# Performance work log

Measured on AMD Instinct MI355X. Metric: run time of the kernel, lower is better.

The kernel has to match this reference:

```python
import jax, jax.numpy as jnp
import numpy as np

WIRES = 4
LAYERS = 3
B = 1024
P = 14 * 14  # 196 patches


def setup_inputs() -> dict:
    key = jax.random.key(0)
    k1, k2, k3 = jax.random.split(key, 3)
    x = jax.random.uniform(k1, (B, 1, 28, 28), jnp.float32)
    q_params = jax.random.normal(k2, (LAYERS, WIRES), jnp.float32)
    W = jax.random.normal(k3, (10, 4 * 14 * 14), jnp.float32) * 0.02
    b = jnp.zeros((10,), jnp.float32)
    return {"x": x, "q_params": q_params, "W": W, "b": b}


def _cnot(state, ctrl, tgt):
    # state: [B,P,2,2,2,2]; wire w lives on axis 2+w
    c_ax, t_ax = 2 + ctrl, 2 + tgt
    s0, s1 = jnp.split(state, 2, axis=c_ax)
    s1 = jnp.flip(s1, axis=t_ax)  # flip target when control=1
    return jnp.concatenate([s0, s1], axis=c_ax)


def _circuit(xp, q_params):
    # xp: [B,P,4] RX angles per wire. Returns <Z_w> per wire: [B,P,4].
    Bn, Pn = xp.shape[0], xp.shape[1]
    state = jnp.zeros((Bn, Pn, 2, 2, 2, 2), jnp.complex64).at[:, :, 0, 0, 0, 0].set(1.0)
    for i in range(LAYERS):
        # RX(x[w]) on each wire (angle varies per batch/patch)
        for w in range(WIRES):
            half = xp[:, :, w] * 0.5
            c = jnp.cos(half).astype(jnp.complex64)
            s = (-1j) * jnp.sin(half).astype(jnp.complex64)
            mat = jnp.stack([jnp.stack([c, s], -1), jnp.stack([s, c], -1)], -2)  # [B,P,2,2]
            st = jnp.moveaxis(state, 2 + w, -1)
            st = jnp.einsum('BPij,BPuvwj->BPuvwi', mat, st)
            state = jnp.moveaxis(st, -1, 2 + w)
        state = _cnot(state, 0, 1)
        state = _cnot(state, 2, 3)
        # RZ(params[i,w]) on each wire (scalar phase, diagonal gate)
        for w in range(WIRES):
            phi = q_params[i, w].astype(jnp.complex64)
            ph = jnp.stack([jnp.exp(-0.5j * phi), jnp.exp(0.5j * phi)])  # [2]
            st = jnp.moveaxis(state, 2 + w, -1) * ph
            state = jnp.moveaxis(st, -1, 2 + w)
    probs = state.real ** 2 + state.imag ** 2  # [B,P,2,2,2,2]
    zs = []
    for w in range(WIRES):
        axes = tuple(a for a in range(2, 6) if a != 2 + w)
        m = probs.sum(axes)  # [B,P,2]
        zs.append(m[..., 0] - m[..., 1])
    return jnp.stack(zs, -1)  # [B,P,4]


def reference(x, q_params, W, b):
    Bn = x.shape[0]
    # 2x2 patches in row-major (r,c) order; per-patch flatten order matches
    # view of x[:,0,r:r+2,c:c+2]: [tl, tr, bl, br]
    xp = x[:, 0].reshape(Bn, 14, 2, 14, 2).transpose(0, 1, 3, 2, 4).reshape(Bn, P, 4)
    z = _circuit(xp, q_params)            # [B,196,4]
    feats = z.reshape(Bn, P * 4).astype(jnp.float32)  # cat order: patch-major, wire-minor
    logits = feats @ W.T + b
    return jax.nn.log_softmax(logits, axis=-1)
```

## Files before the change

kernel.cpp:

```cpp
#include <hip/hip_runtime.h>
#include <math.h>

#define WIRES   4
#define LAYERS  3
#define PATCHES 196

__global__ __launch_bounds__(256) void quanv_fused(
    const float* __restrict__ x,
    const float* __restrict__ qp,
    const float* __restrict__ Wt,
    const float* __restrict__ bias,
    float* __restrict__ out)
{
    __shared__ float phr[LAYERS][16];
    __shared__ float phim[LAYERS][16];
    __shared__ float wsum[4][10];
    __shared__ float lg[10];

    const int b = blockIdx.x;
    const int t = threadIdx.x;

    float cw[4], sw[4];
    if (t < PATCHES) {
        const int r = t / 14, cc = t % 14;
        const float* xb = x + (size_t)b * 784;
        const float2 top = *reinterpret_cast<const float2*>(xb + (2 * r) * 28 + 2 * cc);
        const float2 bot = *reinterpret_cast<const float2*>(xb + (2 * r + 1) * 28 + 2 * cc);
        __sincosf(0.5f * top.x, &sw[0], &cw[0]);
        __sincosf(0.5f * top.y, &sw[1], &cw[1]);
        __sincosf(0.5f * bot.x, &sw[2], &cw[2]);
        __sincosf(0.5f * bot.y, &sw[3], &cw[3]);
    }
    if (t >= 208 && t < 208 + LAYERS * 16) {
        const int idx16 = t - 208;
        const int l = idx16 >> 4, idx = idx16 & 15;
        float th = 0.f;
        #pragma unroll
        for (int w = 0; w < 4; ++w) {
            const float sgn = ((idx >> (3 - w)) & 1) ? 0.5f : -0.5f;
            th += sgn * qp[l * 4 + w];
        }
        float s, c;
        __sincosf(th, &s, &c);
        phr[l][idx]  = c;
        phim[l][idx] = s;
    }
    __syncthreads();

    float z[4] = {0.f, 0.f, 0.f, 0.f};
    if (t < PATCHES) {
        float m01[4], m23[4];
        m01[0] = cw[0] * cw[1]; m01[1] = cw[0] * sw[1];
        m01[2] = sw[0] * cw[1]; m01[3] = sw[0] * sw[1];
        m23[0] = cw[2] * cw[3]; m23[1] = cw[2] * sw[3];
        m23[2] = sw[2] * cw[3]; m23[3] = sw[2] * sw[3];

        float sr[16], si[16];
        #pragma unroll
        for (int i = 0; i < 16; ++i) {
            const float m = m01[i >> 2] * m23[i & 3];
            int ti = (i & 8) ? (i ^ 4) : i;
            ti = (ti & 2) ? (ti ^ 1) : ti;
            const int pc = ((i >> 3) & 1) + ((i >> 2) & 1) + ((i >> 1) & 1) + (i & 1);
            const float pr = phr[0][ti], pi = phim[0][ti];
            float rr, ii;
            switch (pc & 3) {
                case 0: rr =  m * pr; ii =  m * pi; break;
                case 1: rr =  m * pi; ii = -m * pr; break;
                case 2: rr = -m * pr; ii = -m * pi; break;
                default:rr = -m * pi; ii =  m * pr; break;
            }
            sr[ti] = rr; si[ti] = ii;
        }

        #pragma unroll
        for (int l = 1; l < LAYERS; ++l) {
            #pragma unroll
            for (int w = 0; w < 4; ++w) {
                const int m = 8 >> w;
                const float c = cw[w], s = sw[w];
                #pragma unroll
                for (int i = 0; i < 16; ++i) {
                    if (i & m) continue;
                    const int j = i | m;
                    const float a0r = sr[i], a0i = si[i];
                    const float a1r = sr[j], a1i = si[j];
                    sr[i] = fmaf(c, a0r,  s * a1i);
                    si[i] = fmaf(c, a0i, -s * a1r);
                    sr[j] = fmaf(c, a1r,  s * a0i);
                    si[j] = fmaf(c, a1i, -s * a0r);
                }
            }
            #pragma unroll
            for (int i = 0; i < 16; ++i) {
                if ((i & 8) && !(i & 4)) {
                    const int j = i ^ 4;
                    float tr = sr[i]; sr[i] = sr[j]; sr[j] = tr;
                    float ti2 = si[i]; si[i] = si[j]; si[j] = ti2;
                }
            }
            #pragma unroll
            for (int i = 0; i < 16; ++i) {
                if ((i & 2) && !(i & 1)) {
                    const int j = i ^ 1;
                    float tr = sr[i]; sr[i] = sr[j]; sr[j] = tr;
                    float ti2 = si[i]; si[i] = si[j]; si[j] = ti2;
                }
            }
            #pragma unroll
            for (int i = 0; i < 16; ++i) {
                const float pr = phr[l][i], pi = phim[l][i];
                const float rr = sr[i], ii = si[i];
                sr[i] = rr * pr - ii * pi;
                si[i] = rr * pi + ii * pr;
            }
        }

        #pragma unroll
        for (int i = 0; i < 16; ++i) {
            const float p = fmaf(sr[i], sr[i], si[i] * si[i]);
            #pragma unroll
            for (int w = 0; w < 4; ++w)
                z[w] += ((i >> (3 - w)) & 1) ? -p : p;
        }
    }

    float part[10];
    if (t < PATCHES) {
        const float4* W4 = reinterpret_cast<const float4*>(Wt);
        #pragma unroll
        for (int k = 0; k < 10; ++k) {
            const float4 w = W4[k * 196 + t];
            part[k] = fmaf(z[0], w.x, fmaf(z[1], w.y, fmaf(z[2], w.z, z[3] * w.w)));
        }
    } else {
        #pragma unroll
        for (int k = 0; k < 10; ++k) part[k] = 0.f;
    }
    #pragma unroll
    for (int k = 0; k < 10; ++k) {
        #pragma unroll
        for (int off = 32; off > 0; off >>= 1)
            part[k] += __shfl_down(part[k], off, 64);
    }
    const int wave = t >> 6, lane = t & 63;
    if (lane == 0) {
        #pragma unroll
        for (int k = 0; k < 10; ++k) wsum[wave][k] = part[k];
    }
    __syncthreads();
    if (t < 10)
        lg[t] = bias[t] + wsum[0][t] + wsum[1][t] + wsum[2][t] + wsum[3][t];
    __syncthreads();
    if (t < 10) {
        float mx = lg[0];
        #pragma unroll
        for (int k = 1; k < 10; ++k) mx = fmaxf(mx, lg[k]);
        float se = 0.f;
        #pragma unroll
        for (int k = 0; k < 10; ++k) se += expf(lg[k] - mx);
        out[b * 10 + t] = lg[t] - (mx + logf(se));
    }
}

extern "C" void kernel_launch(void* const* d_in, const int* in_sizes, int n_in,
                              void* d_out, int out_size, void* d_ws, size_t ws_size,
                              hipStream_t stream) {
    const float* x    = (const float*)d_in[0];
    const float* qp   = (const float*)d_in[1];
    const float* W    = (const float*)d_in[2];
    const float* bias = (const float*)d_in[3];
    float* out = (float*)d_out;

    const int B = in_sizes[0] / 784;
    quanv_fused<<<B, 256, 0, stream>>>(x, qp, W, bias, out);
}
```

Before: 67.17 us.

## Factor 4-qubit circuit into two independent 2-qubit subsystems

The circuit's CNOTs only couple wires 0-1 and 2-3, so the 16-amplitude state is replaced by two separate 4-amplitude states, evolved independently with pairwise RZ phases computed from sums and differences of the parameters. The per-thread shared-memory phase table and its __syncthreads are removed; every thread now computes the phases itself from the parameters. This removes most of the arithmetic and register pressure in the per-patch circuit simulation, in exchange for redundant per-thread sincos work on the parameters.

```diff
diff --git a/kernel.cpp b/kernel.cpp
--- a/kernel.cpp
+++ b/kernel.cpp
@@ -1,9 +1,44 @@
 #include <hip/hip_runtime.h>
 #include <math.h>
 
-#define WIRES   4
 #define LAYERS  3
 #define PATCHES 196
+
+
+__device__ __forceinline__ void pair_layer(
+    float r[4], float im[4],
+    float cu, float su, float cv, float sv,
+    float cS, float sS, float cD, float sD)
+{
+    {
+        float t0r=r[0], t0i=im[0], t1r=r[2], t1i=im[2];
+        r[0]=fmaf(cu,t0r, su*t1i); im[0]=fmaf(cu,t0i,-su*t1r);
+        r[2]=fmaf(cu,t1r, su*t0i); im[2]=fmaf(cu,t1i,-su*t0r);
+    }
+    {
+        float t0r=r[1], t0i=im[1], t1r=r[3], t1i=im[3];
+        r[1]=fmaf(cu,t0r, su*t1i); im[1]=fmaf(cu,t0i,-su*t1r);
+        r[3]=fmaf(cu,t1r, su*t0i); im[3]=fmaf(cu,t1i,-su*t0r);
+    }
+    {
+        float t0r=r[0], t0i=im[0], t1r=r[1], t1i=im[1];
+        r[0]=fmaf(cv,t0r, sv*t1i); im[0]=fmaf(cv,t0i,-sv*t1r);
+        r[1]=fmaf(cv,t1r, sv*t0i); im[1]=fmaf(cv,t1i,-sv*t0r);
+    }
+    {
+        float t0r=r[2], t0i=im[2], t1r=r[3], t1i=im[3];
+        r[2]=fmaf(cv,t0r, sv*t1i); im[2]=fmaf(cv,t0i,-sv*t1r);
+        r[3]=fmaf(cv,t1r, sv*t0i); im[3]=fmaf(cv,t1i,-sv*t0r);
+    }
+    { float tr=r[2]; r[2]=r[3]; r[3]=tr; float ti=im[2]; im[2]=im[3]; im[3]=ti; }
+    {
+        float rr, ii;
+        rr=r[0]; ii=im[0];  r[0]=fmaf(rr,cS,  ii*sS); im[0]=fmaf(ii,cS, -rr*sS);
+        rr=r[1]; ii=im[1];  r[1]=fmaf(rr,cD,  ii*sD); im[1]=fmaf(ii,cD, -rr*sD);
+        rr=r[2]; ii=im[2];  r[2]=fmaf(rr,cD, -ii*sD); im[2]=fmaf(ii,cD,  rr*sD);
+        rr=r[3]; ii=im[3];  r[3]=fmaf(rr,cS, -ii*sS); im[3]=fmaf(ii,cS,  rr*sS);
+    }
+}
 
 __global__ __launch_bounds__(256) void quanv_fused(
     const float* __restrict__ x,
@@ -12,116 +47,76 @@
     const float* __restrict__ bias,
     float* __restrict__ out)
 {
-    __shared__ float phr[LAYERS][16];
-    __shared__ float phim[LAYERS][16];
     __shared__ float wsum[4][10];
     __shared__ float lg[10];
 
     const int b = blockIdx.x;
     const int t = threadIdx.x;
 
-    float cw[4], sw[4];
+    float cS[LAYERS][2], sS[LAYERS][2], cD[LAYERS][2], sD[LAYERS][2];
+    #pragma unroll
+    for (int l = 0; l < LAYERS; ++l) {
+        #pragma unroll
+        for (int p = 0; p < 2; ++p) {
+            const float pu = qp[l*4 + 2*p], pv = qp[l*4 + 2*p + 1];
+            __sincosf(0.5f*(pu+pv), &sS[l][p], &cS[l][p]);
+            __sincosf(0.5f*(pu-pv), &sD[l][p], &cD[l][p]);
+        }
+    }
+
+    float z[4] = {0.f, 0.f, 0.f, 0.f};
     if (t < PATCHES) {
         const int r = t / 14, cc = t % 14;
         const float* xb = x + (size_t)b * 784;
-        const float2 top = *reinterpret_cast<const float2*>(xb + (2 * r) * 28 + 2 * cc);
-        const float2 bot = *reinterpret_cast<const float2*>(xb + (2 * r + 1) * 28 + 2 * cc);
+        const float2 top = *reinterpret_cast<const float2*>(xb + (2*r)*28 + 2*cc);
+        const float2 bot = *reinterpret_cast<const float2*>(xb + (2*r+1)*28 + 2*cc);
+        float cw[4], sw[4];
         __sincosf(0.5f * top.x, &sw[0], &cw[0]);
         __sincosf(0.5f * top.y, &sw[1], &cw[1]);
         __sincosf(0.5f * bot.x, &sw[2], &cw[2]);
         __sincosf(0.5f * bot.y, &sw[3], &cw[3]);
-    }
-    if (t >= 208 && t < 208 + LAYERS * 16) {
-        const int idx16 = t - 208;
-        const int l = idx16 >> 4, idx = idx16 & 15;
-        float th = 0.f;
-        #pragma unroll
-        for (int w = 0; w < 4; ++w) {
-            const float sgn = ((idx >> (3 - w)) & 1) ? 0.5f : -0.5f;
-            th += sgn * qp[l * 4 + w];
+
+        float Ar[4], Ai[4], Br[4], Bi[4];
+        {
+            const float m0=cw[0]*cw[1], m1=cw[0]*sw[1], m2=sw[0]*cw[1], m3=sw[0]*sw[1];
+            const float cs=cS[0][0], ss=sS[0][0], cd=cD[0][0], sd=sD[0][0];
+            Ar[0]= m0*cs;  Ai[0]=-m0*ss;
+            Ar[1]=-m1*sd;  Ai[1]=-m1*cd;
+            Ar[3]= m2*ss;  Ai[3]=-m2*cs;
+            Ar[2]=-m3*cd;  Ai[2]=-m3*sd;
         }
-        float s, c;
-        __sincosf(th, &s, &c);
-        phr[l][idx]  = c;
-        phim[l][idx] = s;
-    }
-    __syncthreads();
-
-    float z[4] = {0.f, 0.f, 0.f, 0.f};
-    if (t < PATCHES) {
-        float m01[4], m23[4];
-        m01[0] = cw[0] * cw[1]; m01[1] = cw[0] * sw[1];
-        m01[2] = sw[0] * cw[1]; m01[3] = sw[0] * sw[1];
-        m23[0] = cw[2] * cw[3]; m23[1] = cw[2] * sw[3];
-        m23[2] = sw[2] * cw[3]; m23[3] = sw[2] * sw[3];
-
-        float sr[16], si[16];
-        #pragma unroll
-        for (int i = 0; i < 16; ++i) {
-            const float m = m01[i >> 2] * m23[i & 3];
-            int ti = (i & 8) ? (i ^ 4) : i;
-            ti = (ti & 2) ? (ti ^ 1) : ti;
-            const int pc = ((i >> 3) & 1) + ((i >> 2) & 1) + ((i >> 1) & 1) + (i & 1);
-            const float pr = phr[0][ti], pi = phim[0][ti];
-            float rr, ii;
-            switch (pc & 3) {
-                case 0: rr =  m * pr; ii =  m * pi; break;
-                case 1: rr =  m * pi; ii = -m * pr; break;
-                case 2: rr = -m * pr; ii = -m * pi; break;
-                default:rr = -m * pi; ii =  m * pr; break;
-            }
-            sr[ti] = rr; si[ti] = ii;
+        {
+            const float m0=cw[2]*cw[3], m1=cw[2]*sw[3], m2=sw[2]*cw[3], m3=sw[2]*sw[3];
+            const float cs=cS[0][1], ss=sS[0][1], cd=cD[0][1], sd=sD[0][1];
+            Br[0]= m0*cs;  Bi[0]=-m0*ss;
+            Br[1]=-m1*sd;  Bi[1]=-m1*cd;
+            Br[3]= m2*ss;  Bi[3]=-m2*cs;
+            Br[2]=-m3*cd;  Bi[2]=-m3*sd;
         }
 
         #pragma unroll
         for (int l = 1; l < LAYERS; ++l) {
-            #pragma unroll
-            for (int w = 0; w < 4; ++w) {
-                const int m = 8 >> w;
-                const float c = cw[w], s = sw[w];
-                #pragma unroll
-                for (int i = 0; i < 16; ++i) {
-                    if (i & m) continue;
-                    const int j = i | m;
-                    const float a0r = sr[i], a0i = si[i];
-                    const float a1r = sr[j], a1i = si[j];
-                    sr[i] = fmaf(c, a0r,  s * a1i);
-                    si[i] = fmaf(c, a0i, -s * a1r);
-                    sr[j] = fmaf(c, a1r,  s * a0i);
-                    si[j] = fmaf(c, a1i, -s * a0r);
-                }
-            }
-            #pragma unroll
-            for (int i = 0; i < 16; ++i) {
-                if ((i & 8) && !(i & 4)) {
-                    const int j = i ^ 4;
-                    float tr = sr[i]; sr[i] = sr[j]; sr[j] = tr;
-                    float ti2 = si[i]; si[i] = si[j]; si[j] = ti2;
-                }
-            }
-            #pragma unroll
-            for (int i = 0; i < 16; ++i) {
-                if ((i & 2) && !(i & 1)) {
-                    const int j = i ^ 1;
-                    float tr = sr[i]; sr[i] = sr[j]; sr[j] = tr;
-                    float ti2 = si[i]; si[i] = si[j]; si[j] = ti2;
-                }
-            }
-            #pragma unroll
-            for (int i = 0; i < 16; ++i) {
-                const float pr = phr[l][i], pi = phim[l][i];
-                const float rr = sr[i], ii = si[i];
-                sr[i] = rr * pr - ii * pi;
-                si[i] = rr * pi + ii * pr;
-            }
+            pair_layer(Ar, Ai, cw[0],sw[0], cw[1],sw[1],
+                       cS[l][0],sS[l][0], cD[l][0],sD[l][0]);
+            pair_layer(Br, Bi, cw[2],sw[2], cw[3],sw[3],
+                       cS[l][1],sS[l][1], cD[l][1],sD[l][1]);
         }
 
-        #pragma unroll
-        for (int i = 0; i < 16; ++i) {
-            const float p = fmaf(sr[i], sr[i], si[i] * si[i]);
-            #pragma unroll
-            for (int w = 0; w < 4; ++w)
-                z[w] += ((i >> (3 - w)) & 1) ? -p : p;
+        {
+            const float p0=fmaf(Ar[0],Ar[0],Ai[0]*Ai[0]);
+            const float p1=fmaf(Ar[1],Ar[1],Ai[1]*Ai[1]);
+            const float p2=fmaf(Ar[2],Ar[2],Ai[2]*Ai[2]);
+            const float p3=fmaf(Ar[3],Ar[3],Ai[3]*Ai[3]);
+            z[0] = (p0+p1) - (p2+p3);
+            z[1] = (p0+p2) - (p1+p3);
+        }
+        {
+            const float p0=fmaf(Br[0],Br[0],Bi[0]*Bi[0]);
+            const float p1=fmaf(Br[1],Br[1],Bi[1]*Bi[1]);
+            const float p2=fmaf(Br[2],Br[2],Bi[2]*Bi[2]);
+            const float p3=fmaf(Br[3],Br[3],Bi[3]*Bi[3]);
+            z[2] = (p0+p1) - (p2+p3);
+            z[3] = (p0+p2) - (p1+p3);
         }
     }
 
```

After: 64.36 us. 4.2% less time.
